# Kernel tuning notes

Hardware: AMD Instinct MI355X
Metric: run time of the kernel (lower is better)

## Reference

```python
import jax, jax.numpy as jnp
import numpy as np

N_BLOCKS, B0, B1 = 128, 8, 8
OUT = N_BLOCKS * B0   # 1024
IN = N_BLOCKS * B1    # 1024 (cond_dim = None)
BATCH = 16384


def _masks():
    # block_diag_mask / block_tril_mask from flowjax (structural int32 constants)
    diag = np.zeros((OUT, IN), np.int32)
    tril = np.zeros((OUT, IN), np.int32)
    for i in range(N_BLOCKS):
        diag[i * B0:(i + 1) * B0, i * B1:(i + 1) * B1] = 1
        tril[(i + 1) * B0:, i * B1:(i + 1) * B1] = 1
    return jnp.asarray(diag), jnp.asarray(tril)


def setup_inputs() -> dict:
    key = jax.random.key(0)
    kx, kw, kb, ks = jax.random.split(key, 4)
    b_diag_mask, b_tril_mask = _masks()
    limit = float(np.sqrt(6.0 / (OUT + IN)))  # glorot_uniform
    W = jax.random.uniform(kw, (OUT, IN), jnp.float32, -limit, limit) * (b_diag_mask + b_tril_mask)
    bias = (jax.random.uniform(kb, (OUT,), jnp.float32) - 0.5) * (2.0 / np.sqrt(OUT))
    W_log_scale = jnp.log(jax.random.uniform(ks, (OUT, 1), jnp.float32, 1e-3, 1.0))
    x = jax.random.normal(kx, (BATCH, IN), jnp.float32)
    return {"x": x, "W": W, "bias": bias, "W_log_scale": W_log_scale,
            "b_diag_mask": b_diag_mask, "b_tril_mask": b_tril_mask}


def reference(x, W, bias, W_log_scale, b_diag_mask, b_tril_mask):
    # weight normalisation: exp() on diag blocks, identity on strictly-lower blocks,
    # per-row L2 norm, then learned scale
    Wm = jnp.exp(W) * b_diag_mask + W * b_tril_mask            # [OUT, IN]
    W_norms = jnp.linalg.norm(Wm, axis=-1, keepdims=True)      # [OUT, 1]
    Wn = jnp.exp(W_log_scale) * Wm / W_norms                   # [OUT, IN]
    # batched block-triangular matvec (vmap of W @ x + bias over batch)
    y = x @ Wn.T + bias                                        # [BATCH, OUT]
    # gather diagonal blocks -> (n_blocks, B0, B1), same row-major order as
    # jnp.where(b_diag_mask) indexing in the original
    idx = jnp.arange(N_BLOCKS)
    jac_3d = Wn.reshape(N_BLOCKS, B0, N_BLOCKS, B1)[idx, :, idx, :]  # [N_BLOCKS, B0, B1]
    return y, jnp.log(jac_3d)
```

## Files before the change

kernel.cpp:

```cpp
#include <hip/hip_runtime.h>

#define IN_DIM   1024
#define OUT_DIM  1024
#define BATCH    16384

#define BM 128
#define BN 256
#define BK 32
#define RS 32
#define BUFE 24576

typedef __attribute__((ext_vector_type(8))) short          bf16x8;
typedef __attribute__((ext_vector_type(8))) unsigned short u16x8;
typedef __attribute__((ext_vector_type(4))) unsigned short u16x4;
typedef __attribute__((ext_vector_type(4))) float          f32x4;

__device__ __forceinline__ unsigned short f2bf(float f) {
    unsigned u = __float_as_uint(f);
    u += 0x7FFFu + ((u >> 16) & 1u);
    return (unsigned short)(u >> 16);
}
__device__ __forceinline__ float bf2f(unsigned short h) {
    return __uint_as_float((unsigned)h << 16);
}

#define GLOAD_LDS16(g, l)                                                      \
    __builtin_amdgcn_global_load_lds(                                          \
        (const __attribute__((address_space(1))) unsigned int*)(g),            \
        (__attribute__((address_space(3))) unsigned int*)(l), 16, 0, 0)

__global__ __launch_bounds__(256) void prep_kernel(
    const float* __restrict__ W, const float* __restrict__ wls,
    unsigned short* __restrict__ wh, unsigned short* __restrict__ wl,
    float* __restrict__ jac)
{
    const int warp = threadIdx.x >> 6;
    const int lane = threadIdx.x & 63;
    const int row  = blockIdx.x * 4 + warp;
    const int r    = row >> 3;
    const int d0   = r * 8;
    const int nk   = d0 + 8;
    const float* Wr = W + (size_t)row * IN_DIM;

    float ss = 0.f;
    for (int k = lane * 4; k < nk; k += 256) {
        float4 v = *(const float4*)&Wr[k];
        if (k >= d0) { v.x = expf(v.x); v.y = expf(v.y); v.z = expf(v.z); v.w = expf(v.w); }
        ss += v.x * v.x + v.y * v.y + v.z * v.z + v.w * v.w;
    }
    #pragma unroll
    for (int off = 32; off >= 1; off >>= 1) ss += __shfl_xor(ss, off);

    const float lscale = wls[row] - 0.5f * logf(ss);
    const float scale  = expf(lscale);

    for (int k = lane * 4; k < IN_DIM; k += 256) {
        float4 v = {0.f, 0.f, 0.f, 0.f};
        if (k < nk) {
            v = *(const float4*)&Wr[k];
            if (k >= d0) { v.x = expf(v.x); v.y = expf(v.y); v.z = expf(v.z); v.w = expf(v.w); }
            v.x *= scale; v.y *= scale; v.z *= scale; v.w *= scale;
        }
        u16x4 h, l;
        const float f[4] = {v.x, v.y, v.z, v.w};
        #pragma unroll
        for (int i = 0; i < 4; ++i) {
            h[i] = f2bf(f[i]);
            l[i] = f2bf(f[i] - bf2f(h[i]));
        }
        *(u16x4*)&wh[(size_t)row * IN_DIM + k] = h;
        *(u16x4*)&wl[(size_t)row * IN_DIM + k] = l;
    }
    if (lane < 8) jac[r * 64 + (row & 7) * 8 + lane] = lscale + Wr[d0 + lane];
}

__global__ __launch_bounds__(512, 2) void gemm_kernel(
    const float* __restrict__ x,
    const unsigned short* __restrict__ wh, const unsigned short* __restrict__ wl,
    const float* __restrict__ bias, float* __restrict__ y)
{
    __shared__ __align__(16) unsigned short smem[2 * BUFE];

    const int bid = (int)blockIdx.x;
    const int seg = bid >> 7;
    const int sb  = bid & 127;
    const int nt  = 3 - seg;
    const int mt  = (sb & 7) * 16 + (sb >> 3);
    const int m0  = mt * BM;
    const int n0  = nt * BN;
    const int Klim = n0 + BN;

    const int t    = threadIdx.x;
    const int lane = t & 63;
    const int wid  = t >> 6;
    const int wr   = wid >> 2;
    const int wc   = wid & 3;

    const int sxr = t >> 2;
    const int sxc = (t & 3) * 8;
    const float* xg = x + (size_t)(m0 + sxr) * IN_DIM + sxc;

    const unsigned short* whg = wh + (size_t)(n0 + wid * 32 + (lane >> 2)) * IN_DIM + (lane & 3) * 8;
    const unsigned short* wlg = wl + (size_t)(n0 + wid * 32 + (lane >> 2)) * IN_DIM + (lane & 3) * 8;

    const int fl = lane & 15;
    const int fk = (lane >> 4) * 8;
    const int a_base = (wr * 64 + fl) * RS + fk;
    const int b_base = (wc * 64 + fl) * RS + fk;

    f32x4 acc[4][4];
    #pragma unroll
    for (int i = 0; i < 4; ++i)
        #pragma unroll
        for (int j = 0; j < 4; ++j) acc[i][j] = (f32x4){0.f, 0.f, 0.f, 0.f};

    float4 xva, xvb;

    auto LOAD_X = [&](int k0) {
        xva = *(const float4*)(xg + k0);
        xvb = *(const float4*)(xg + k0 + 4);
    };
    auto STAGE_W = [&](int b, int k0) {
        unsigned short* whp = smem + b * BUFE + 2 * BM * RS;
        unsigned short* wlp = whp + BN * RS;
        const unsigned short* gh = whg + k0;
        const unsigned short* gl = wlg + k0;
        GLOAD_LDS16(gh,                whp + wid * 1024);
        GLOAD_LDS16(gh + 16 * IN_DIM,  whp + wid * 1024 + 512);
        GLOAD_LDS16(gl,                wlp + wid * 1024);
        GLOAD_LDS16(gl + 16 * IN_DIM,  wlp + wid * 1024 + 512);
    };
    auto CVT_X = [&](int b) {
        unsigned short* xhp = smem + b * BUFE;
        unsigned short* xlp = xhp + BM * RS;
        const float f[8] = {xva.x, xva.y, xva.z, xva.w, xvb.x, xvb.y, xvb.z, xvb.w};
        u16x8 h, l;
        #pragma unroll
        for (int i = 0; i < 8; ++i) {
            h[i] = f2bf(f[i]);
            l[i] = f2bf(f[i] - bf2f(h[i]));
        }
        *(u16x8*)&xhp[sxr * RS + sxc] = h;
        *(u16x8*)&xlp[sxr * RS + sxc] = l;
    };
    auto COMPUTE = [&](int b) {
        const unsigned short* xhp = smem + b * BUFE;
        const unsigned short* xlp = xhp + BM * RS;
        const unsigned short* whp = xlp + BM * RS;
        const unsigned short* wlp = whp + BN * RS;
        bf16x8 bh[4], bl[4];
        #pragma unroll
        for (int fc = 0; fc < 4; ++fc) {
            bh[fc] = *(const bf16x8*)&whp[b_base + fc * 16 * RS];
            bl[fc] = *(const bf16x8*)&wlp[b_base + fc * 16 * RS];
        }
        #pragma unroll
        for (int fr = 0; fr < 4; ++fr) {
            const bf16x8 ah = *(const bf16x8*)&xhp[a_base + fr * 16 * RS];
            const bf16x8 al = *(const bf16x8*)&xlp[a_base + fr * 16 * RS];
            #pragma unroll
            for (int fc = 0; fc < 4; ++fc) {
                acc[fr][fc] = __builtin_amdgcn_mfma_f32_16x16x32_bf16(ah, bh[fc], acc[fr][fc], 0, 0, 0);
                acc[fr][fc] = __builtin_amdgcn_mfma_f32_16x16x32_bf16(ah, bl[fc], acc[fr][fc], 0, 0, 0);
                acc[fr][fc] = __builtin_amdgcn_mfma_f32_16x16x32_bf16(al, bh[fc], acc[fr][fc], 0, 0, 0);
            }
        }
    };

    LOAD_X(0);
    STAGE_W(0, 0);
    CVT_X(0);
    __syncthreads();

    int cur = 0;
    for (int k0 = 0; k0 < Klim; k0 += BK) {
        const bool more = (k0 + BK) < Klim;
        if (more) {
            LOAD_X(k0 + BK);
            STAGE_W(cur ^ 1, k0 + BK);
        }
        COMPUTE(cur);
        if (more) CVT_X(cur ^ 1);
        __syncthreads();
        cur ^= 1;
    }

    float* yt = (float*)smem;
    const int erow = t >> 2;
    const int ec0  = (t & 3) * 4;
    #pragma unroll
    for (int h = 0; h < 2; ++h) {
        if ((wc >> 1) == h) {
            #pragma unroll
            for (int fr = 0; fr < 4; ++fr) {
                const int row0 = wr * 64 + fr * 16 + (lane >> 4) * 4;
                #pragma unroll
                for (int fc = 0; fc < 4; ++fc) {
                    const int col = (wc & 1) * 64 + fc * 16 + fl;
                    #pragma unroll
                    for (int i = 0; i < 4; ++i)
                        yt[(row0 + i) * 132 + col] = acc[fr][fc][i];
                }
            }
        }
        __syncthreads();
        #pragma unroll
        for (int j = 0; j < 8; ++j) {
            const int col = ec0 + j * 16;
            float4 v = *(const float4*)&yt[erow * 132 + col];
            const float4 bb = *(const float4*)&bias[n0 + h * 128 + col];
            v.x += bb.x; v.y += bb.y; v.z += bb.z; v.w += bb.w;
            *(float4*)&y[(size_t)(m0 + erow) * OUT_DIM + n0 + h * 128 + col] = v;
        }
        __syncthreads();
    }
}

extern "C" void kernel_launch(void* const* d_in, const int* in_sizes, int n_in,
                              void* d_out, int out_size, void* d_ws, size_t ws_size,
                              hipStream_t stream)
{
    const float* x    = (const float*)d_in[0];
    const float* W    = (const float*)d_in[1];
    const float* bias = (const float*)d_in[2];
    const float* wls  = (const float*)d_in[3];

    unsigned short* wh = (unsigned short*)d_ws;
    unsigned short* wl = wh + (size_t)OUT_DIM * IN_DIM;
    float* y   = (float*)d_out;
    float* jac = y + (size_t)BATCH * OUT_DIM;

    prep_kernel<<<OUT_DIM / 4, 256, 0, stream>>>(W, wls, wh, wl, jac);

    gemm_kernel<<<4 * 128, 512, 0, stream>>>(x, wh, wl, bias, y);
}
```

Before: 180.8 us.

## Triple-buffer weight staging and use fragment-ordered LDS layout with lgkm-only barriers

Weight tiles are now staged two steps ahead into a three-slot LDS ring, while x keeps a double buffer. LDS tiles are stored in MFMA-fragment order, so each lane reads one contiguous 16-byte chunk instead of a padded row-stride layout. The loop barrier waits only on LDS/lgkm counters rather than doing a full __syncthreads, so global-to-LDS loads can stay in flight across iterations. The aim is to hide more load latency and cut bank conflicts, at the cost of 128KB of LDS per block, which may lower occupancy below the launch bound of 2 blocks.

```diff
diff --git a/kernel.cpp b/kernel.cpp
--- a/kernel.cpp
+++ b/kernel.cpp
@@ -7,8 +7,6 @@
 #define BM 128
 #define BN 256
 #define BK 32
-#define RS 32
-#define BUFE 24576
 
 typedef __attribute__((ext_vector_type(8))) short          bf16x8;
 typedef __attribute__((ext_vector_type(8))) unsigned short u16x8;
@@ -28,6 +26,14 @@
     __builtin_amdgcn_global_load_lds(                                          \
         (const __attribute__((address_space(1))) unsigned int*)(g),            \
         (__attribute__((address_space(3))) unsigned int*)(l), 16, 0, 0)
+
+#define LGKM_BARRIER()                                                         \
+    do {                                                                       \
+        asm volatile("s_waitcnt lgkmcnt(0)" ::: "memory");                     \
+        __builtin_amdgcn_sched_barrier(0);                                     \
+        __builtin_amdgcn_s_barrier();                                          \
+        __builtin_amdgcn_sched_barrier(0);                                     \
+    } while (0)
 
 __global__ __launch_bounds__(256) void prep_kernel(
     const float* __restrict__ W, const float* __restrict__ wls,
@@ -79,7 +85,7 @@
     const unsigned short* __restrict__ wh, const unsigned short* __restrict__ wl,
     const float* __restrict__ bias, float* __restrict__ y)
 {
-    __shared__ __align__(16) unsigned short smem[2 * BUFE];
+    __shared__ __align__(16) unsigned short smem[65536];
 
     const int bid = (int)blockIdx.x;
     const int seg = bid >> 7;
@@ -88,25 +94,24 @@
     const int mt  = (sb & 7) * 16 + (sb >> 3);
     const int m0  = mt * BM;
     const int n0  = nt * BN;
-    const int Klim = n0 + BN;
+    const int nsteps = (n0 + BN) >> 5;
 
     const int t    = threadIdx.x;
     const int lane = t & 63;
     const int wid  = t >> 6;
     const int wr   = wid >> 2;
     const int wc   = wid & 3;
-
-    const int sxr = t >> 2;
-    const int sxc = (t & 3) * 8;
-    const float* xg = x + (size_t)(m0 + sxr) * IN_DIM + sxc;
-
-    const unsigned short* whg = wh + (size_t)(n0 + wid * 32 + (lane >> 2)) * IN_DIM + (lane & 3) * 8;
-    const unsigned short* wlg = wl + (size_t)(n0 + wid * 32 + (lane >> 2)) * IN_DIM + (lane & 3) * 8;
-
-    const int fl = lane & 15;
-    const int fk = (lane >> 4) * 8;
-    const int a_base = (wr * 64 + fl) * RS + fk;
-    const int b_base = (wc * 64 + fl) * RS + fk;
+    const int lr   = lane & 15;
+    const int lq   = lane >> 4;
+
+    const float* xg = x + (size_t)(m0 + wid * 16 + lr) * IN_DIM + lq * 8;
+
+    const size_t wsrc = (size_t)(n0 + wid * 32 + lr) * IN_DIM + lq * 8;
+    const unsigned short* whg = wh + wsrc;
+    const unsigned short* wlg = wl + wsrc;
+
+    unsigned short* const xs  = smem;
+    unsigned short* const wsm = smem + 16384;
 
     f32x4 acc[4][4];
     #pragma unroll
@@ -121,18 +126,15 @@
         xvb = *(const float4*)(xg + k0 + 4);
     };
     auto STAGE_W = [&](int b, int k0) {
-        unsigned short* whp = smem + b * BUFE + 2 * BM * RS;
-        unsigned short* wlp = whp + BN * RS;
-        const unsigned short* gh = whg + k0;
-        const unsigned short* gl = wlg + k0;
-        GLOAD_LDS16(gh,                whp + wid * 1024);
-        GLOAD_LDS16(gh + 16 * IN_DIM,  whp + wid * 1024 + 512);
-        GLOAD_LDS16(gl,                wlp + wid * 1024);
-        GLOAD_LDS16(gl + 16 * IN_DIM,  wlp + wid * 1024 + 512);
+        unsigned short* dh = wsm + b * 16384 + wid * 1024;
+        unsigned short* dl = dh + 8192;
+        GLOAD_LDS16(whg + k0,                dh);
+        GLOAD_LDS16(whg + k0 + 16 * IN_DIM,  dh + 512);
+        GLOAD_LDS16(wlg + k0,                dl);
+        GLOAD_LDS16(wlg + k0 + 16 * IN_DIM,  dl + 512);
     };
     auto CVT_X = [&](int b) {
-        unsigned short* xhp = smem + b * BUFE;
-        unsigned short* xlp = xhp + BM * RS;
+        unsigned short* dh = xs + b * 8192;
         const float f[8] = {xva.x, xva.y, xva.z, xva.w, xvb.x, xvb.y, xvb.z, xvb.w};
         u16x8 h, l;
         #pragma unroll
@@ -140,24 +142,26 @@
             h[i] = f2bf(f[i]);
             l[i] = f2bf(f[i] - bf2f(h[i]));
         }
-        *(u16x8*)&xhp[sxr * RS + sxc] = h;
-        *(u16x8*)&xlp[sxr * RS + sxc] = l;
-    };
-    auto COMPUTE = [&](int b) {
-        const unsigned short* xhp = smem + b * BUFE;
-        const unsigned short* xlp = xhp + BM * RS;
-        const unsigned short* whp = xlp + BM * RS;
-        const unsigned short* wlp = whp + BN * RS;
+        *(u16x8*)&dh[t * 8]        = h;
+        *(u16x8*)&dh[4096 + t * 8] = l;
+    };
+    auto COMPUTE = [&](int xb, int wbuf) {
+        const unsigned short* xh_ = xs + xb * 8192;
+        const unsigned short* xl_ = xh_ + 4096;
+        const unsigned short* wh_ = wsm + wbuf * 16384;
+        const unsigned short* wl_ = wh_ + 8192;
+        const int ao = wr * 2048 + lane * 8;
+        const int bo = wc * 2048 + lane * 8;
         bf16x8 bh[4], bl[4];
         #pragma unroll
         for (int fc = 0; fc < 4; ++fc) {
-            bh[fc] = *(const bf16x8*)&whp[b_base + fc * 16 * RS];
-            bl[fc] = *(const bf16x8*)&wlp[b_base + fc * 16 * RS];
+            bh[fc] = *(const bf16x8*)&wh_[bo + fc * 512];
+            bl[fc] = *(const bf16x8*)&wl_[bo + fc * 512];
         }
         #pragma unroll
         for (int fr = 0; fr < 4; ++fr) {
-            const bf16x8 ah = *(const bf16x8*)&xhp[a_base + fr * 16 * RS];
-            const bf16x8 al = *(const bf16x8*)&xlp[a_base + fr * 16 * RS];
+            const bf16x8 ah = *(const bf16x8*)&xh_[ao + fr * 512];
+            const bf16x8 al = *(const bf16x8*)&xl_[ao + fr * 512];
             #pragma unroll
             for (int fc = 0; fc < 4; ++fc) {
                 acc[fr][fc] = __builtin_amdgcn_mfma_f32_16x16x32_bf16(ah, bh[fc], acc[fr][fc], 0, 0, 0);
@@ -167,23 +171,31 @@
         }
     };
 
+    STAGE_W(0, 0);
     LOAD_X(0);
-    STAGE_W(0, 0);
+    STAGE_W(1, BK);
     CVT_X(0);
+    LGKM_BARRIER();
+
+    int xb = 0, wb = 0, wb2 = 2;
+    int k0 = 0;
+    for (int i = 0; i < nsteps; ++i, k0 += BK) {
+        const bool has1 = (i + 1) < nsteps;
+        const bool has2 = (i + 2) < nsteps;
+        if (has1) LOAD_X(k0 + BK);
+        if (has2) {
+            STAGE_W(wb2, k0 + 2 * BK);
+            wb2 = (wb2 == 2) ? 0 : wb2 + 1;
+        }
+        COMPUTE(xb, wb);
+        wb = (wb == 2) ? 0 : wb + 1;
+        if (has1) {
+            CVT_X(xb ^ 1);
+            LGKM_BARRIER();
+            xb ^= 1;
+        }
+    }
     __syncthreads();
-
-    int cur = 0;
-    for (int k0 = 0; k0 < Klim; k0 += BK) {
-        const bool more = (k0 + BK) < Klim;
-        if (more) {
-            LOAD_X(k0 + BK);
-            STAGE_W(cur ^ 1, k0 + BK);
-        }
-        COMPUTE(cur);
-        if (more) CVT_X(cur ^ 1);
-        __syncthreads();
-        cur ^= 1;
-    }
 
     float* yt = (float*)smem;
     const int erow = t >> 2;
@@ -193,10 +205,10 @@
         if ((wc >> 1) == h) {
             #pragma unroll
             for (int fr = 0; fr < 4; ++fr) {
-                const int row0 = wr * 64 + fr * 16 + (lane >> 4) * 4;
+                const int row0 = wr * 64 + fr * 16 + lq * 4;
                 #pragma unroll
                 for (int fc = 0; fc < 4; ++fc) {
-                    const int col = (wc & 1) * 64 + fc * 16 + fl;
+                    const int col = (wc & 1) * 64 + fc * 16 + lr;
                     #pragma unroll
                     for (int i = 0; i < 4; ++i)
                         yt[(row0 + i) * 132 + col] = acc[fr][fc][i];
```

After: 201.4 us. 1.11x slower.
